# Kernel optimization log

Hardware: AMD Instinct MI355X
Metric: run time of the kernel (lower is better)

## Reference

```python
import jax, jax.numpy as jnp
import numpy as np

B, C, H, W = 64, 512, 32, 32
D = C // 8  # 64


def setup_inputs() -> dict:
    key = jax.random.key(0)
    k1, k2, k3, k4 = jax.random.split(key, 4)
    x = jax.random.normal(k1, (B, C, H, W), dtype=jnp.float32)
    query_m = jax.random.normal(k2, (H * W, D), dtype=jnp.float32)
    key_m = jax.random.normal(k3, (H * W, D), dtype=jnp.float32)
    # 1x1 conv C->C: weight [C_out, C_in], kaiming-ish scale
    value_w = jax.random.normal(k4, (C, C), dtype=jnp.float32) * (1.0 / np.sqrt(C))
    value_b = jnp.zeros((C,), dtype=jnp.float32)
    return {"x": x, "query_m": query_m, "key_m": key_m,
            "value_w": value_w, "value_b": value_b}


def reference(x, query_m, key_m, value_w, value_b):
    b, c, h, w = x.shape
    xf = x.reshape(b, c, h * w)                        # [B, C, N]
    q = jnp.einsum('bcn,nd->bcd', xf, query_m)         # [B, C, D]
    k = jnp.einsum('bcn,nd->bcd', xf, key_m)           # [B, C, D]
    energy = jnp.einsum('bcd,bed->bce', q, k)          # [B, C, C]
    energy = jax.nn.sigmoid(energy)
    attention = jax.nn.softmax(energy, axis=-2)        # softmax over rows (dim=-2)
    # 1x1 conv = channel matmul + bias
    v = jnp.einsum('bcn,oc->bon', xf, value_w) + value_b[None, :, None]  # [B, C, N]
    # out[b,j,n] = sum_i v[b,i,n] * attention[b,i,j]
    out = jnp.einsum('bin,bij->bjn', v, attention)     # [B, C, N]
    return out.reshape(b, c, h, w)
```

## Files before the change

### kernel.cpp

```cpp
#include <hip/hip_runtime.h>

#define BK 32

typedef __attribute__((ext_vector_type(8))) short bf16x8;
typedef __attribute__((ext_vector_type(4))) float f32x4;

__device__ __forceinline__ unsigned short f2bf(float f) {
  unsigned u = __builtin_bit_cast(unsigned, f);
  unsigned r = (u + 0x7FFFu + ((u >> 16) & 1u)) >> 16;
  return (unsigned short)r;
}
__device__ __forceinline__ float bf2f(unsigned short h) {
  return __builtin_bit_cast(float, (unsigned)h << 16);
}
__device__ __forceinline__ unsigned pack2(unsigned short a, unsigned short b) {
  return (unsigned)a | ((unsigned)b << 16);
}

__device__ __forceinline__ void gld_lds16(const void* g, void* l) {
  __builtin_amdgcn_global_load_lds(
      (const __attribute__((address_space(1))) unsigned int*)g,
      (__attribute__((address_space(3))) unsigned int*)l, 16, 0, 0);
}

#define SCHED0() __builtin_amdgcn_sched_barrier(0)
#define NTBAR() do { SCHED0(); __builtin_amdgcn_s_barrier(); SCHED0(); } while (0)
#define VMW(N) do { asm volatile("s_waitcnt vmcnt(" #N ")" ::: "memory"); SCHED0(); } while (0)
#define LGKM0() do { asm volatile("s_waitcnt lgkmcnt(0)" ::: "memory"); SCHED0(); } while (0)
#define MFMA16(a, b, c) __builtin_amdgcn_mfma_f32_16x16x32_bf16(a, b, c, 0, 0, 0)

__device__ __forceinline__ void split8_store(float4 v0, float4 v1,
                                             unsigned short* Hdst,
                                             unsigned short* Ldst) {
  float f[8] = {v0.x, v0.y, v0.z, v0.w, v1.x, v1.y, v1.z, v1.w};
  unsigned short hh[8], ll[8];
#pragma unroll
  for (int i = 0; i < 8; ++i) {
    hh[i] = f2bf(f[i]);
    ll[i] = f2bf(f[i] - bf2f(hh[i]));
  }
  *reinterpret_cast<uint4*>(Hdst) = make_uint4(pack2(hh[0], hh[1]), pack2(hh[2], hh[3]),
                                               pack2(hh[4], hh[5]), pack2(hh[6], hh[7]));
  *reinterpret_cast<uint4*>(Ldst) = make_uint4(pack2(ll[0], ll[1]), pack2(ll[2], ll[3]),
                                               pack2(ll[4], ll[5]), pack2(ll[6], ll[7]));
}

__global__ __launch_bounds__(256) void qkm_split(const float* __restrict__ Qm,
                                                 const float* __restrict__ Km,
                                                 unsigned short* __restrict__ Th,
                                                 unsigned short* __restrict__ Tl) {
  __shared__ float lt[64][65];
  int k0 = blockIdx.x * 64;
  int half = blockIdx.y;
  const float* M = half ? Km : Qm;
  int t = threadIdx.x;
  int cl = (t & 15) * 4;
  int rl = t >> 4;
#pragma unroll
  for (int rr = 0; rr < 4; ++rr) {
    int r = rl + rr * 16;
    float4 v = *reinterpret_cast<const float4*>(&M[(long)(k0 + r) * 64 + cl]);
    lt[cl + 0][r] = v.x;
    lt[cl + 1][r] = v.y;
    lt[cl + 2][r] = v.z;
    lt[cl + 3][r] = v.w;
  }
  __syncthreads();
#pragma unroll
  for (int rr = 0; rr < 4; ++rr) {
    int c = rl + rr * 16;
    unsigned short h[4], lo[4];
#pragma unroll
    for (int i = 0; i < 4; ++i) {
      float f = lt[c][cl + i];
      h[i] = f2bf(f);
      lo[i] = f2bf(f - bf2f(h[i]));
    }
    *reinterpret_cast<uint2*>(&Th[(long)(half * 64 + c) * 1024 + k0 + cl]) =
        make_uint2(pack2(h[0], h[1]), pack2(h[2], h[3]));
    *reinterpret_cast<uint2*>(&Tl[(long)(half * 64 + c) * 1024 + k0 + cl]) =
        make_uint2(pack2(lo[0], lo[1]), pack2(lo[2], lo[3]));
  }
}

__global__ __launch_bounds__(256) void k1_mfma(const float* __restrict__ x,
                                               const unsigned short* __restrict__ Th,
                                               const unsigned short* __restrict__ Tl,
                                               float* __restrict__ qk) {
  __shared__ unsigned short Dh[2][128 * 32];
  __shared__ unsigned short Dl[2][128 * 32];
  __shared__ unsigned short Xh[2][64 * 32];
  __shared__ unsigned short Xl[2][64 * 32];
  const int t = threadIdx.x;
  const int l = t & 63;
  const int w = t >> 6;
  const int wr = w >> 1, wc = w & 1;
  const long mBase = (long)blockIdx.x * 64;

  f32x4 acc[4][2];
#pragma unroll
  for (int m = 0; m < 4; ++m)
#pragma unroll
    for (int n = 0; n < 2; ++n) acc[m][n] = (f32x4){0.f, 0.f, 0.f, 0.f};

  const int xrow_l = t >> 2;
  const int kslot = t & 3;
  const int xsl = kslot ^ ((t >> 3) & 3);
  const int srcslot = (l & 3) ^ ((l >> 3) & 3);
  const int frag_off = (l & 15) * 32 + ((((l >> 4) ^ (l >> 1)) & 3) * 8);
  const float* xrow = x + (mBase + xrow_l) * 1024;

#define K1_STAGE_B(k0, p)                                                     \
  {                                                                           \
    _Pragma("unroll") for (int c = 0; c < 2; ++c) {                           \
      int ch = c * 4 + w;                                                     \
      int row = ch * 16 + (l >> 2);                                           \
      gld_lds16(Th + (long)row * 1024 + (k0) + srcslot * 8, &Dh[p][ch * 512]);\
      gld_lds16(Tl + (long)row * 1024 + (k0) + srcslot * 8, &Dl[p][ch * 512]);\
    }                                                                         \
  }

#define K1_COMPUTE(p)                                                         \
  {                                                                           \
    bf16x8 dh[4], dl[4], xh[2], xl[2];                                        \
    _Pragma("unroll") for (int m = 0; m < 4; ++m) {                           \
      dh[m] = *reinterpret_cast<const bf16x8*>(&Dh[p][(wr * 64 + m * 16) * 32 + frag_off]); \
      dl[m] = *reinterpret_cast<const bf16x8*>(&Dl[p][(wr * 64 + m * 16) * 32 + frag_off]); \
    }                                                                         \
    _Pragma("unroll") for (int n = 0; n < 2; ++n) {                           \
      xh[n] = *reinterpret_cast<const bf16x8*>(&Xh[p][(wc * 32 + n * 16) * 32 + frag_off]); \
      xl[n] = *reinterpret_cast<const bf16x8*>(&Xl[p][(wc * 32 + n * 16) * 32 + frag_off]); \
    }                                                                         \
    _Pragma("unroll") for (int m = 0; m < 4; ++m)                             \
        _Pragma("unroll") for (int n = 0; n < 2; ++n) {                       \
      acc[m][n] = MFMA16(dh[m], xh[n], acc[m][n]);                            \
      acc[m][n] = MFMA16(dh[m], xl[n], acc[m][n]);                            \
      acc[m][n] = MFMA16(dl[m], xh[n], acc[m][n]);                            \
    }                                                                         \
  }

  {
    float4 p0 = *reinterpret_cast<const float4*>(&xrow[kslot * 8]);
    float4 p1 = *reinterpret_cast<const float4*>(&xrow[kslot * 8 + 4]);
    K1_STAGE_B(0, 0);
    split8_store(p0, p1, &Xh[0][xrow_l * 32 + xsl * 8], &Xl[0][xrow_l * 32 + xsl * 8]);
  }

  for (int k0 = 0; k0 < 1024; k0 += 64) {
    __syncthreads();
    float4 na0 = *reinterpret_cast<const float4*>(&xrow[k0 + 32 + kslot * 8]);
    float4 na1 = *reinterpret_cast<const float4*>(&xrow[k0 + 32 + kslot * 8 + 4]);
    K1_STAGE_B(k0 + 32, 1);
    K1_COMPUTE(0);
    split8_store(na0, na1, &Xh[1][xrow_l * 32 + xsl * 8], &Xl[1][xrow_l * 32 + xsl * 8]);
    __syncthreads();
    if (k0 + 64 < 1024) {
      float4 nb0 = *reinterpret_cast<const float4*>(&xrow[k0 + 64 + kslot * 8]);
      float4 nb1 = *reinterpret_cast<const float4*>(&xrow[k0 + 64 + kslot * 8 + 4]);
      K1_STAGE_B(k0 + 64, 0);
      K1_COMPUTE(1);
      split8_store(nb0, nb1, &Xh[0][xrow_l * 32 + xsl * 8], &Xl[0][xrow_l * 32 + xsl * 8]);
    } else {
      K1_COMPUTE(1);
    }
  }

#pragma unroll
  for (int m = 0; m < 4; ++m)
#pragma unroll
    for (int n = 0; n < 2; ++n) {
      int d0 = wr * 64 + m * 16 + (l >> 4) * 4;
      long xr = mBase + wc * 32 + n * 16 + (l & 15);
      *reinterpret_cast<float4*>(&qk[xr * 128 + d0]) =
          make_float4(acc[m][n][0], acc[m][n][1], acc[m][n][2], acc[m][n][3]);
    }
#undef K1_STAGE_B
#undef K1_COMPUTE
}

__global__ __launch_bounds__(256) void k2a_mfma(const float* __restrict__ qk,
                                                unsigned short* __restrict__ st) {
  __shared__ unsigned short Ah[128 * 64];
  __shared__ unsigned short Al[128 * 64];
  __shared__ unsigned short Bh[128 * 64];
  __shared__ unsigned short Bl[128 * 64];
  const int t = threadIdx.x;
  const int l = t & 63;
  const int w = t >> 6;
  const int wr = w >> 1, wc = w & 1;

  const int cpx = gridDim.x >> 3;
  const int orig = blockIdx.x;
  const int lw = (orig & 7) * cpx + (orig >> 3);
  const int b = lw >> 4;
  const int tile = lw & 15;
  const int iBase = (tile >> 2) * 128;
  const int jBase = (tile & 3) * 128;
  const float* qb = qk + (long)b * 512 * 128;

  {
    const int r = t >> 1;
    const int kh = t & 1;
    const float* qa = &qb[(long)(iBase + r) * 128 + kh * 32];
    const float* kb = &qb[(long)(jBase + r) * 128 + 64 + kh * 32];
#pragma unroll
    for (int c = 0; c < 4; ++c) {
      int s = (kh * 4 + c) ^ (r & 7);
      float4 a0 = *reinterpret_cast<const float4*>(&qa[c * 8]);
      float4 a1 = *reinterpret_cast<const float4*>(&qa[c * 8 + 4]);
      split8_store(a0, a1, &Ah[r * 64 + s * 8], &Al[r * 64 + s * 8]);
      float4 b0 = *reinterpret_cast<const float4*>(&kb[c * 8]);
      float4 b1 = *reinterpret_cast<const float4*>(&kb[c * 8 + 4]);
      split8_store(b0, b1, &Bh[r * 64 + s * 8], &Bl[r * 64 + s * 8]);
    }
  }
  __syncthreads();

  f32x4 acc[4][4];
#pragma unroll
  for (int m = 0; m < 4; ++m)
#pragma unroll
    for (int n = 0; n < 4; ++n) acc[m][n] = (f32x4){0.f, 0.f, 0.f, 0.f};

#pragma unroll
  for (int ks = 0; ks < 2; ++ks) {
    bf16x8 ah[4], al4[4], bh[4], bl4[4];
#pragma unroll
    for (int m = 0; m < 4; ++m) {
      int row = wr * 64 + m * 16 + (l & 15);
      int off = row * 64 + ((ks * 4 + (l >> 4)) ^ (row & 7)) * 8;
      ah[m] = *reinterpret_cast<const bf16x8*>(&Ah[off]);
      al4[m] = *reinterpret_cast<const bf16x8*>(&Al[off]);
    }
#pragma unroll
    for (int n = 0; n < 4; ++n) {
      int row = wc * 64 + n * 16 + (l & 15);
      int off = row * 64 + ((ks * 4 + (l >> 4)) ^ (row & 7)) * 8;
      bh[n] = *reinterpret_cast<const bf16x8*>(&Bh[off]);
      bl4[n] = *reinterpret_cast<const bf16x8*>(&Bl[off]);
    }
#pragma unroll
    for (int m = 0; m < 4; ++m)
#pragma unroll
      for (int n = 0; n < 4; ++n) {
        acc[m][n] = MFMA16(ah[m], bh[n], acc[m][n]);
        acc[m][n] = MFMA16(ah[m], bl4[n], acc[m][n]);
        acc[m][n] = MFMA16(al4[m], bh[n], acc[m][n]);
      }
  }

  unsigned short* sb = st + (long)b * 512 * 512;
#pragma unroll
  for (int m = 0; m < 4; ++m)
#pragma unroll
    for (int n = 0; n < 4; ++n) {
      int i0 = iBase + wr * 64 + m * 16 + (l >> 4) * 4;
      int j = jBase + wc * 64 + n * 16 + (l & 15);
      unsigned short p[4];
#pragma unroll
      for (int reg = 0; reg < 4; ++reg) {
        float sg = 1.0f / (1.0f + __expf(-acc[m][n][reg]));
        p[reg] = f2bf(__expf(sg));
      }
      *reinterpret_cast<uint2*>(&sb[(long)j * 512 + i0]) = *reinterpret_cast<uint2*>(p);
    }
}

__global__ __launch_bounds__(256) void k2b_rsum(const unsigned short* __restrict__ st,
                                                const float* __restrict__ bias,
                                                float* __restrict__ rsum,
                                                float* __restrict__ attbias) {
  int jg = blockIdx.x * 4 + (threadIdx.x >> 6);
  int l = threadIdx.x & 63;
  const unsigned short* row = st + (long)jg * 512 + l * 8;
  ushort4 u0 = *reinterpret_cast<const ushort4*>(row);
  ushort4 u1 = *reinterpret_cast<const ushort4*>(row + 4);
  float4 b0 = *reinterpret_cast<const float4*>(&bias[l * 8]);
  float4 b1 = *reinterpret_cast<const float4*>(&bias[l * 8 + 4]);
  float f0 = bf2f(u0.x), f1 = bf2f(u0.y), f2 = bf2f(u0.z), f3 = bf2f(u0.w);
  float f4 = bf2f(u1.x), f5 = bf2f(u1.y), f6 = bf2f(u1.z), f7 = bf2f(u1.w);
  float sum = (f0 + f1) + (f2 + f3) + ((f4 + f5) + (f6 + f7));
  float sumb = f0 * b0.x + f1 * b0.y + f2 * b0.z + f3 * b0.w +
               f4 * b1.x + f5 * b1.y + f6 * b1.z + f7 * b1.w;
#pragma unroll
  for (int off = 32; off > 0; off >>= 1) {
    sum += __shfl_down(sum, off);
    sumb += __shfl_down(sumb, off);
  }
  if (l == 0) {
    float r = 1.0f / sum;
    rsum[jg] = r;
    attbias[jg] = sumb * r;
  }
}

__global__ __launch_bounds__(256) void transpose_conv(const float* __restrict__ in,
                                                      unsigned short* __restrict__ out,
                                                      int inRows, int inCols,
                                                      long inBatch, long outBatch) {
  __shared__ unsigned short lt[64][65];
  int b = blockIdx.z;
  int r0 = blockIdx.y * 64;
  int c0 = blockIdx.x * 64;
  const float* I = in + (long)b * inBatch;
  unsigned short* O = out + (long)b * outBatch;
  int t = threadIdx.x;
  int cl = (t & 15) * 4;
  int rl = t >> 4;
#pragma unroll
  for (int rr = 0; rr < 4; ++rr) {
    int r = rl + rr * 16;
    float4 v = *reinterpret_cast<const float4*>(&I[(long)(r0 + r) * inCols + c0 + cl]);
    lt[cl + 0][r] = f2bf(v.x);
    lt[cl + 1][r] = f2bf(v.y);
    lt[cl + 2][r] = f2bf(v.z);
    lt[cl + 3][r] = f2bf(v.w);
  }
  __syncthreads();
#pragma unroll
  for (int rr = 0; rr < 4; ++rr) {
    int c = rl + rr * 16;
    unsigned short v[4] = {lt[c][cl], lt[c][cl + 1], lt[c][cl + 2], lt[c][cl + 3]};
    *reinterpret_cast<uint2*>(&O[(long)(c0 + c) * inRows + r0 + cl]) =
        *reinterpret_cast<uint2*>(&v[0]);
  }
}

template <int MODE>
__global__ __launch_bounds__(512) void mfma_nt256(const unsigned short* __restrict__ Abase,
                                                  const unsigned short* __restrict__ Bbase,
                                                  const float* __restrict__ rowscale,
                                                  unsigned short* __restrict__ Wout,
                                                  float* __restrict__ Fout) {
  __shared__ unsigned short As[2][256 * 64];
  __shared__ unsigned short Bs[2][256 * 64];
  const int t = threadIdx.x;
  const int l = t & 63;
  const int w = t >> 6;
  const int wr = w >> 2;
  const int wc = w & 3;

  const int cpx = gridDim.x >> 3;
  const int orig = blockIdx.x;
  const int lw = (orig & 7) * cpx + (orig >> 3);
  const int TPB_SH = (MODE == 0) ? 2 : 3;
  const int b = lw >> TPB_SH;
  const int tile = lw & ((1 << TPB_SH) - 1);
  const int mBase = (tile >> 1) * 256;
  const int nBase = (tile & 1) * 256;

  const unsigned short* Ag = Abase + ((MODE == 0) ? 0L : (long)b * (1024 * 512)) + (long)mBase * 512;
  const unsigned short* Bg = Bbase + (long)b * (512 * 512) + (long)nBase * 512;

  f32x4 acc[8][4];
#pragma unroll
  for (int m = 0; m < 8; ++m)
#pragma unroll
    for (int n = 0; n < 4; ++n) acc[m][n] = (f32x4){0.f, 0.f, 0.f, 0.f};

  const int srcslot = (l & 7) ^ (l >> 3);
  const int so0 = ((l >> 4) ^ (l & 7)) * 8;
  const int so1 = ((4 + (l >> 4)) ^ (l & 7)) * 8;

#define STG_A(p, tt, pr)                                                       \
  gld_lds16(Ag + (long)((pr) * 64 + w * 8 + (l >> 3)) * 512 + (tt) * 64 + srcslot * 8, \
            &As[p][((pr) * 64 + w * 8) * 64]);
#define STG_B(p, tt, pr)                                                       \
  gld_lds16(Bg + (long)((pr) * 64 + w * 8 + (l >> 3)) * 512 + (tt) * 64 + srcslot * 8, \
            &Bs[p][((pr) * 64 + w * 8) * 64]);

#define PHASE(p, q, STAGE_STMT, VMSTMT)                                        \
  {                                                                            \
    bf16x8 a00 = *reinterpret_cast<const bf16x8*>(                             \
        &As[p][(wr * 128 + (2 * (q)) * 16 + (l & 15)) * 64 + so0]);            \
    bf16x8 a01 = *reinterpret_cast<const bf16x8*>(                             \
        &As[p][(wr * 128 + (2 * (q)) * 16 + (l & 15)) * 64 + so1]);            \
    bf16x8 a10 = *reinterpret_cast<const bf16x8*>(                             \
        &As[p][(wr * 128 + (2 * (q) + 1) * 16 + (l & 15)) * 64 + so0]);        \
    bf16x8 a11 = *reinterpret_cast<const bf16x8*>(                             \
        &As[p][(wr * 128 + (2 * (q) + 1) * 16 + (l & 15)) * 64 + so1]);        \
    if ((q) == 0) {                                                            \
      _Pragma("unroll") for (int n = 0; n < 4; ++n) {                          \
        bfr0[n] = *reinterpret_cast<const bf16x8*>(                            \
            &Bs[p][(wc * 64 + n * 16 + (l & 15)) * 64 + so0]);                 \
        bfr1[n] = *reinterpret_cast<const bf16x8*>(                            \
            &Bs[p][(wc * 64 + n * 16 + (l & 15)) * 64 + so1]);                 \
      }                                                                        \
    }                                                                          \
    STAGE_STMT;                                                                \
    SCHED0();                                                                  \
    __builtin_amdgcn_s_barrier();                                              \
    LGKM0();                                                                   \
    __builtin_amdgcn_s_setprio(1);                                             \
    _Pragma("unroll") for (int n = 0; n < 4; ++n) {                            \
      acc[2 * (q)][n] = MFMA16(a00, bfr0[n], acc[2 * (q)][n]);                 \
      acc[2 * (q)][n] = MFMA16(a01, bfr1[n], acc[2 * (q)][n]);                 \
      acc[2 * (q) + 1][n] = MFMA16(a10, bfr0[n], acc[2 * (q) + 1][n]);         \
      acc[2 * (q) + 1][n] = MFMA16(a11, bfr1[n], acc[2 * (q) + 1][n]);         \
    }                                                                          \
    __builtin_amdgcn_s_setprio(0);                                             \
    VMSTMT;                                                                    \
    NTBAR();                                                                   \
  }

  bf16x8 bfr0[4], bfr1[4];

  STG_A(0, 0, 0); STG_A(0, 0, 1); STG_A(0, 0, 2); STG_A(0, 0, 3);
  STG_B(0, 0, 0); STG_B(0, 0, 1); STG_B(0, 0, 2); STG_B(0, 0, 3);
  STG_B(1, 1, 0); STG_B(1, 1, 1); STG_B(1, 1, 2); STG_B(1, 1, 3);
  STG_A(1, 1, 0); STG_A(1, 1, 2);
  VMW(6);
  NTBAR();

  for (int it = 0; it < 4; ++it) {
    const int t1 = 2 * it + 1;
    const int t2 = (2 * it + 2 < 8) ? 2 * it + 2 : 7;
    const int t3 = (2 * it + 3 < 8) ? 2 * it + 3 : 7;
    PHASE(0, 0, { STG_A(1, t1, 1); STG_A(1, t1, 3); }, );
    PHASE(0, 1, { STG_B(0, t2, 0); STG_B(0, t2, 1); }, VMW(10));
    PHASE(0, 2, { STG_B(0, t2, 2); STG_B(0, t2, 3); }, );
    PHASE(0, 3, { STG_A(0, t2, 0); STG_A(0, t2, 2); }, VMW(8));
    PHASE(1, 0, { STG_A(0, t2, 1); STG_A(0, t2, 3); }, );
    PHASE(1, 1, { STG_B(1, t3, 0); STG_B(1, t3, 1); }, VMW(10));
    PHASE(1, 2, { STG_B(1, t3, 2); STG_B(1, t3, 3); }, );
    PHASE(1, 3, { STG_A(1, t3, 0); STG_A(1, t3, 2); }, VMW(8));
  }
#undef PHASE
#undef STG_A
#undef STG_B

  if (MODE == 0) {
    unsigned short* W = Wout + (long)b * (512 * 512);
#pragma unroll
    for (int n = 0; n < 4; ++n) {
      int j = nBase + wc * 64 + n * 16 + (l & 15);
      float rs = rowscale[b * 512 + j];
#pragma unroll
      for (int m = 0; m < 8; ++m) {
        int c0 = mBase + wr * 128 + m * 16 + (l >> 4) * 4;
        unsigned short p[4];
#pragma unroll
        for (int reg = 0; reg < 4; ++reg) p[reg] = f2bf(acc[m][n][reg] * rs);
        *reinterpret_cast<uint2*>(&W[(long)j * 512 + c0]) = *reinterpret_cast<uint2*>(p);
      }
    }
  } else {
    float* O = Fout + (long)b * (512 * 1024);
#pragma unroll
    for (int n = 0; n < 4; ++n) {
      int j = nBase + wc * 64 + n * 16 + (l & 15);
      float ab = rowscale[b * 512 + j];
#pragma unroll
      for (int m = 0; m < 8; ++m) {
        int n0 = mBase + wr * 128 + m * 16 + (l >> 4) * 4;
        *reinterpret_cast<float4*>(&O[(long)j * 1024 + n0]) =
            make_float4(acc[m][n][0] + ab, acc[m][n][1] + ab,
                        acc[m][n][2] + ab, acc[m][n][3] + ab);
      }
    }
  }
}

extern "C" void kernel_launch(void* const* d_in, const int* in_sizes, int n_in,
                              void* d_out, int out_size, void* d_ws, size_t ws_size,
                              hipStream_t stream) {
  const float* x  = (const float*)d_in[0];
  const float* Qm = (const float*)d_in[1];
  const float* Km = (const float*)d_in[2];
  const float* vw = (const float*)d_in[3];
  const float* vb = (const float*)d_in[4];
  float* out = (float*)d_out;

  float* ws = (float*)d_ws;
  float* qk = ws;
  unsigned short* st   = (unsigned short*)(ws + 4194304);
  unsigned short* weff = (unsigned short*)(ws + 4194304 + 8388608);
  unsigned short* xbT  = (unsigned short*)(ws + 4194304 + 16777216);
  unsigned short* vwT  = (unsigned short*)(ws + 4194304 + 33554432);
  unsigned short* qkTh = (unsigned short*)(ws + 4194304 + 33554432 + 131072);
  unsigned short* qkTl = qkTh + 131072;
  float* rsum    = ws + 4194304 + 33554432 + 131072 + 131072;
  float* attbias = rsum + 32768;

  transpose_conv<<<dim3(16, 8, 64), 256, 0, stream>>>(x, xbT, 512, 1024, 524288L, 524288L);
  transpose_conv<<<dim3(8, 8, 1), 256, 0, stream>>>(vw, vwT, 512, 512, 0L, 0L);
  qkm_split<<<dim3(16, 2), 256, 0, stream>>>(Qm, Km, qkTh, qkTl);
  k1_mfma<<<512, 256, 0, stream>>>(x, qkTh, qkTl, qk);
  k2a_mfma<<<1024, 256, 0, stream>>>(qk, st);
  k2b_rsum<<<8192, 256, 0, stream>>>(st, vb, rsum, attbias);
  mfma_nt256<0><<<256, 512, 0, stream>>>(vwT, st, rsum, weff, nullptr);
  mfma_nt256<1><<<512, 512, 0, stream>>>(xbT, weff, attbias, nullptr, out);
}
```

Measured before the change: 212.7 us.

## Fuse x transpose into k1 and emit pre-split bf16 qk for k2a

The separate transpose_conv pass over x is removed. k1_mfma now writes the transposed bf16-high x tile (xbT) from its shared-memory staging buffers while it computes q/k. k1 also stores q/k as bf16 hi/lo pairs, so k2a can load them directly into LDS with global_load_lds instead of reading fp32 and splitting per tile. This avoids a full extra read of x (128 MB) and the repeated split work in k2a, at the cost of extra LDS reads and global writes inside k1's main loop.

```diff
diff --git a/kernel.cpp b/kernel.cpp
--- a/kernel.cpp
+++ b/kernel.cpp
@@ -86,7 +86,9 @@
 __global__ __launch_bounds__(256) void k1_mfma(const float* __restrict__ x,
                                                const unsigned short* __restrict__ Th,
                                                const unsigned short* __restrict__ Tl,
-                                               float* __restrict__ qk) {
+                                               unsigned short* __restrict__ qkh,
+                                               unsigned short* __restrict__ qkl,
+                                               unsigned short* __restrict__ xbT) {
   __shared__ unsigned short Dh[2][128 * 32];
   __shared__ unsigned short Dl[2][128 * 32];
   __shared__ unsigned short Xh[2][64 * 32];
@@ -96,6 +98,8 @@
   const int w = t >> 6;
   const int wr = w >> 1, wc = w & 1;
   const long mBase = (long)blockIdx.x * 64;
+  const int b = blockIdx.x >> 3;
+  const int cBase = (blockIdx.x & 7) * 64;
 
   f32x4 acc[4][2];
 #pragma unroll
@@ -139,6 +143,22 @@
     }                                                                         \
   }
 
+#define K1_WRITEBACK(p, kk)                                                   \
+  {                                                                           \
+    int n_loc = t >> 3;                                                       \
+    int c0w = (t & 7) * 8;                                                    \
+    unsigned short vv[8];                                                     \
+    _Pragma("unroll") for (int i2 = 0; i2 < 8; ++i2) {                        \
+      int r = c0w + i2;                                                       \
+      int sl2 = (n_loc >> 3) ^ ((r >> 1) & 3);                                \
+      vv[i2] = Xh[p][r * 32 + sl2 * 8 + (n_loc & 7)];                         \
+    }                                                                         \
+    *reinterpret_cast<uint4*>(                                                \
+        &xbT[(long)b * 524288 + (long)((kk) + n_loc) * 512 + cBase + c0w]) =  \
+        make_uint4(pack2(vv[0], vv[1]), pack2(vv[2], vv[3]),                  \
+                   pack2(vv[4], vv[5]), pack2(vv[6], vv[7]));                 \
+  }
+
   {
     float4 p0 = *reinterpret_cast<const float4*>(&xrow[kslot * 8]);
     float4 p1 = *reinterpret_cast<const float4*>(&xrow[kslot * 8 + 4]);
@@ -153,6 +173,7 @@
     K1_STAGE_B(k0 + 32, 1);
     K1_COMPUTE(0);
     split8_store(na0, na1, &Xh[1][xrow_l * 32 + xsl * 8], &Xl[1][xrow_l * 32 + xsl * 8]);
+    K1_WRITEBACK(0, k0);
     __syncthreads();
     if (k0 + 64 < 1024) {
       float4 nb0 = *reinterpret_cast<const float4*>(&xrow[k0 + 64 + kslot * 8]);
@@ -160,8 +181,10 @@
       K1_STAGE_B(k0 + 64, 0);
       K1_COMPUTE(1);
       split8_store(nb0, nb1, &Xh[0][xrow_l * 32 + xsl * 8], &Xl[0][xrow_l * 32 + xsl * 8]);
+      K1_WRITEBACK(1, k0 + 32);
     } else {
       K1_COMPUTE(1);
+      K1_WRITEBACK(1, k0 + 32);
     }
   }
 
@@ -171,14 +194,25 @@
     for (int n = 0; n < 2; ++n) {
       int d0 = wr * 64 + m * 16 + (l >> 4) * 4;
       long xr = mBase + wc * 32 + n * 16 + (l & 15);
-      *reinterpret_cast<float4*>(&qk[xr * 128 + d0]) =
-          make_float4(acc[m][n][0], acc[m][n][1], acc[m][n][2], acc[m][n][3]);
+      unsigned short h4[4], l4[4];
+#pragma unroll
+      for (int reg = 0; reg < 4; ++reg) {
+        float v = acc[m][n][reg];
+        h4[reg] = f2bf(v);
+        l4[reg] = f2bf(v - bf2f(h4[reg]));
+      }
+      *reinterpret_cast<uint2*>(&qkh[xr * 128 + d0]) =
+          make_uint2(pack2(h4[0], h4[1]), pack2(h4[2], h4[3]));
+      *reinterpret_cast<uint2*>(&qkl[xr * 128 + d0]) =
+          make_uint2(pack2(l4[0], l4[1]), pack2(l4[2], l4[3]));
     }
 #undef K1_STAGE_B
 #undef K1_COMPUTE
-}
-
-__global__ __launch_bounds__(256) void k2a_mfma(const float* __restrict__ qk,
+#undef K1_WRITEBACK
+}
+
+__global__ __launch_bounds__(256) void k2a_mfma(const unsigned short* __restrict__ qkh,
+                                                const unsigned short* __restrict__ qkl,
                                                 unsigned short* __restrict__ st) {
   __shared__ unsigned short Ah[128 * 64];
   __shared__ unsigned short Al[128 * 64];
@@ -196,23 +230,18 @@
   const int tile = lw & 15;
   const int iBase = (tile >> 2) * 128;
   const int jBase = (tile & 3) * 128;
-  const float* qb = qk + (long)b * 512 * 128;
-
-  {
-    const int r = t >> 1;
-    const int kh = t & 1;
-    const float* qa = &qb[(long)(iBase + r) * 128 + kh * 32];
-    const float* kb = &qb[(long)(jBase + r) * 128 + 64 + kh * 32];
-#pragma unroll
-    for (int c = 0; c < 4; ++c) {
-      int s = (kh * 4 + c) ^ (r & 7);
-      float4 a0 = *reinterpret_cast<const float4*>(&qa[c * 8]);
-      float4 a1 = *reinterpret_cast<const float4*>(&qa[c * 8 + 4]);
-      split8_store(a0, a1, &Ah[r * 64 + s * 8], &Al[r * 64 + s * 8]);
-      float4 b0 = *reinterpret_cast<const float4*>(&kb[c * 8]);
-      float4 b1 = *reinterpret_cast<const float4*>(&kb[c * 8 + 4]);
-      split8_store(b0, b1, &Bh[r * 64 + s * 8], &Bl[r * 64 + s * 8]);
-    }
+  const long bq = (long)b * 512;
+
+  const int sg = (l & 7) ^ (l >> 3);
+#pragma unroll
+  for (int c4 = 0; c4 < 4; ++c4) {
+    int rb = w * 32 + c4 * 8;
+    long rowA = bq + iBase + rb + (l >> 3);
+    long rowB = bq + jBase + rb + (l >> 3);
+    gld_lds16(qkh + rowA * 128 + sg * 8, &Ah[rb * 64]);
+    gld_lds16(qkl + rowA * 128 + sg * 8, &Al[rb * 64]);
+    gld_lds16(qkh + rowB * 128 + 64 + sg * 8, &Bh[rb * 64]);
+    gld_lds16(qkl + rowB * 128 + 64 + sg * 8, &Bl[rb * 64]);
   }
   __syncthreads();
 
@@ -259,8 +288,8 @@
       unsigned short p[4];
 #pragma unroll
       for (int reg = 0; reg < 4; ++reg) {
-        float sg = 1.0f / (1.0f + __expf(-acc[m][n][reg]));
-        p[reg] = f2bf(__expf(sg));
+        float sg2 = 1.0f / (1.0f + __expf(-acc[m][n][reg]));
+        p[reg] = f2bf(__expf(sg2));
       }
       *reinterpret_cast<uint2*>(&sb[(long)j * 512 + i0]) = *reinterpret_cast<uint2*>(p);
     }
@@ -472,7 +501,8 @@
   float* out = (float*)d_out;
 
   float* ws = (float*)d_ws;
-  float* qk = ws;
+  unsigned short* qkh  = (unsigned short*)ws;
+  unsigned short* qkl  = qkh + 4194304;
   unsigned short* st   = (unsigned short*)(ws + 4194304);
   unsigned short* weff = (unsigned short*)(ws + 4194304 + 8388608);
   unsigned short* xbT  = (unsigned short*)(ws + 4194304 + 16777216);
@@ -482,11 +512,10 @@
   float* rsum    = ws + 4194304 + 33554432 + 131072 + 131072;
   float* attbias = rsum + 32768;
 
-  transpose_conv<<<dim3(16, 8, 64), 256, 0, stream>>>(x, xbT, 512, 1024, 524288L, 524288L);
   transpose_conv<<<dim3(8, 8, 1), 256, 0, stream>>>(vw, vwT, 512, 512, 0L, 0L);
   qkm_split<<<dim3(16, 2), 256, 0, stream>>>(Qm, Km, qkTh, qkTl);
-  k1_mfma<<<512, 256, 0, stream>>>(x, qkTh, qkTl, qk);
-  k2a_mfma<<<1024, 256, 0, stream>>>(qk, st);
+  k1_mfma<<<512, 256, 0, stream>>>(x, qkTh, qkTl, qkh, qkl, xbT);
+  k2a_mfma<<<1024, 256, 0, stream>>>(qkh, qkl, st);
   k2b_rsum<<<8192, 256, 0, stream>>>(st, vb, rsum, attbias);
   mfma_nt256<0><<<256, 512, 0, stream>>>(vwT, st, rsum, weff, nullptr);
   mfma_nt256<1><<<512, 512, 0, stream>>>(xbT, weff, attbias, nullptr, out);
```

New measurement: 204.8 us. 1.04x faster.
